# Kernel tuning notes

Measured on AMD Instinct MI355X. Metric: run time of the kernel, lower is better.

The kernel has to match this reference:

```python
import jax, jax.numpy as jnp
import numpy as np


def maxpool2x2(x):
    # NCHW 2x2 max pool, stride 2
    return jax.lax.reduce_window(x, -jnp.inf, jax.lax.max, (1, 1, 2, 2), (1, 1, 2, 2), 'VALID')


def _xavier_uniform(k, shape):
    fan_out, fan_in = shape
    lim = np.sqrt(6.0 / (fan_in + fan_out))
    return jax.random.uniform(k, shape, jnp.float32, -lim, lim)


def setup_inputs() -> dict:
    key = jax.random.key(0)
    ks = jax.random.split(key, 5)
    C = 64
    x = jax.random.normal(ks[0], (4, C, 128, 128), jnp.float32)
    Wq = _xavier_uniform(ks[1], (C // 8, C))  # 1x1 conv == channel matmul
    Wk = _xavier_uniform(ks[2], (C // 8, C))
    Wv = _xavier_uniform(ks[3], (C // 2, C))
    Wo = _xavier_uniform(ks[4], (C, C // 2))
    gamma = jnp.full((1,), 0.1, jnp.float32)  # nonzero so attention branch contributes
    return {"x": x, "Wq": Wq, "Wk": Wk, "Wv": Wv, "Wo": Wo, "gamma": gamma}


def reference(x, Wq, Wk, Wv, Wo, gamma):
    b, c, w, h = x.shape
    # 1x1 convs as channel contractions
    q = jnp.einsum('oc,bchw->bohw', Wq, x).reshape(b, c // 8, w * h)          # [b, c/8, k]
    k_ = maxpool2x2(jnp.einsum('oc,bchw->bohw', Wk, x)).reshape(b, c // 8, -1)  # [b, c/8, f]
    v = maxpool2x2(jnp.einsum('oc,bchw->bohw', Wv, x)).reshape(b, c // 2, -1)   # [b, c/2, f]
    # softmax over full-resolution query positions k (last axis), per pooled position f
    weights = jax.nn.softmax(jnp.einsum('bcf,bck->bfk', k_, q), axis=-1)        # [b, f, k]
    out = jnp.einsum('bcf,bfk->bck', v, weights).reshape(b, c // 2, w, h)       # [b, c/2, w, h]
    out = jnp.einsum('oc,bchw->bohw', Wo, out)                                   # [b, c, w, h]
    return gamma * out + x
```

## Files before the change

### kernel.cpp

```cpp
#include <hip/hip_runtime.h>
#include <cstdint>
#include <cstddef>


#define LOG2E 1.44269504088896340736f

typedef __attribute__((ext_vector_type(8)))  __bf16 bf8_t;
typedef __attribute__((ext_vector_type(16))) float  fx16;

__device__ __forceinline__ unsigned short f2bf(float f) {
  unsigned int u = __builtin_bit_cast(unsigned int, f);
  u += 0x7FFFu + ((u >> 16) & 1u);
  return (unsigned short)(u >> 16);
}
__device__ __forceinline__ unsigned int pk2(unsigned short lo, unsigned short hi) {
  return (unsigned int)lo | ((unsigned int)hi << 16);
}
__device__ __forceinline__ int pi16(int s) {
  int m = (s >> 2) & 3;
  return (m == 1 || m == 2) ? (s ^ 12) : s;
}

#if __has_builtin(__builtin_amdgcn_exp2f)
#define EXP2F __builtin_amdgcn_exp2f
#else
#define EXP2F exp2f
#endif

__global__ void __launch_bounds__(256) k_qkv(const float* __restrict__ x,
                                             const float* __restrict__ Wq,
                                             const float* __restrict__ Wk,
                                             const float* __restrict__ Wv,
                                             unsigned short* __restrict__ Qp,
                                             unsigned short* __restrict__ KpB,
                                             float* __restrict__ Vp) {
  __shared__ float wq[64][8], wk[64][8], wv[64][32];
  int t = threadIdx.x;
  for (int i = t; i < 512; i += 256) {
    wq[i & 63][i >> 6] = Wq[i];
    wk[i & 63][i >> 6] = Wk[i];
  }
  for (int i = t; i < 2048; i += 256) wv[i & 63][i >> 6] = Wv[i];
  __syncthreads();
  int gid = blockIdx.x * 256 + t;
  int b = gid >> 14, r = gid & 16383, f = r >> 2, pos = r & 3;
  int p0 = ((f >> 6) << 1) | (pos >> 1);
  int p1 = ((f & 63) << 1) | (pos & 1);
  int k = p0 * 128 + p1;
  const float* xp = x + (size_t)b * (64 * 16384) + k;
  float q[8], kc[8], vc[32];
#pragma unroll
  for (int o = 0; o < 8; ++o) { q[o] = 0.f; kc[o] = 0.f; }
#pragma unroll
  for (int o = 0; o < 32; ++o) vc[o] = 0.f;
  for (int c = 0; c < 64; ++c) {
    float xv = xp[(size_t)c * 16384];
    const float4* q4 = reinterpret_cast<const float4*>(&wq[c][0]);
    const float4* k4 = reinterpret_cast<const float4*>(&wk[c][0]);
    const float4* v4 = reinterpret_cast<const float4*>(&wv[c][0]);
#pragma unroll
    for (int j = 0; j < 2; ++j) {
      float4 a = q4[j], bq = k4[j];
      q[4 * j]      += a.x * xv; q[4 * j + 1]  += a.y * xv;
      q[4 * j + 2]  += a.z * xv; q[4 * j + 3]  += a.w * xv;
      kc[4 * j]     += bq.x * xv; kc[4 * j + 1] += bq.y * xv;
      kc[4 * j + 2] += bq.z * xv; kc[4 * j + 3] += bq.w * xv;
    }
#pragma unroll
    for (int j = 0; j < 8; ++j) {
      float4 a = v4[j];
      vc[4 * j]     += a.x * xv; vc[4 * j + 1] += a.y * xv;
      vc[4 * j + 2] += a.z * xv; vc[4 * j + 3] += a.w * xv;
    }
  }
  unsigned short q16[8];
#pragma unroll
  for (int o = 0; o < 8; ++o) q16[o] = f2bf(q[o]);
  uint4 qa, z4;
  qa.x = pk2(q16[0], q16[1]); qa.y = pk2(q16[2], q16[3]);
  qa.z = pk2(q16[4], q16[5]); qa.w = pk2(q16[6], q16[7]);
  z4.x = z4.y = z4.z = z4.w = 0u;
  uint4* qdst = reinterpret_cast<uint4*>(Qp + ((size_t)b * 16384 + k) * 16);
  qdst[0] = qa; qdst[1] = z4;
#pragma unroll
  for (int o = 0; o < 8; ++o) {
    kc[o] = fmaxf(kc[o], __shfl_xor(kc[o], 1));
    kc[o] = fmaxf(kc[o], __shfl_xor(kc[o], 2));
  }
#pragma unroll
  for (int o = 0; o < 32; ++o) {
    vc[o] = fmaxf(vc[o], __shfl_xor(vc[o], 1));
    vc[o] = fmaxf(vc[o], __shfl_xor(vc[o], 2));
  }
  if (pos == 0) {
    size_t idx = (size_t)b * 4096 + f;
    unsigned short k16[8];
#pragma unroll
    for (int o = 0; o < 8; ++o) k16[o] = f2bf(kc[o] * LOG2E);
    uint4 ka;
    ka.x = pk2(k16[0], k16[1]); ka.y = pk2(k16[2], k16[3]);
    ka.z = pk2(k16[4], k16[5]); ka.w = pk2(k16[6], k16[7]);
    uint4* kdst = reinterpret_cast<uint4*>(KpB + idx * 16);
    kdst[0] = ka; kdst[1] = z4;
    float4* vdst = reinterpret_cast<float4*>(Vp + idx * 32);
#pragma unroll
    for (int j = 0; j < 8; ++j)
      vdst[j] = make_float4(vc[4 * j], vc[4 * j + 1], vc[4 * j + 2], vc[4 * j + 3]);
  }
}

__global__ void __launch_bounds__(1024) k_lsum(const unsigned short* __restrict__ Qp,
                                               const unsigned short* __restrict__ KpB,
                                               float* __restrict__ Ls) {
  int b = blockIdx.x >> 6, g = blockIdx.x & 63;
  int wv = threadIdx.x >> 6, lane = threadIdx.x & 63;
  int half = lane >> 5, l31 = lane & 31;
  const unsigned short* kb =
      KpB + ((size_t)(b * 4096 + g * 64 + l31)) * 16 + half * 8;
  bf8_t A0 = *reinterpret_cast<const bf8_t*>(kb);
  bf8_t A1 = *reinterpret_cast<const bf8_t*>(kb + 32 * 16);
  const unsigned short* qbase = Qp + ((size_t)b * 16384) * 16 + half * 8;
  fx16 z;
#pragma unroll
  for (int i = 0; i < 16; ++i) z[i] = 0.f;
  float l[32];
#pragma unroll
  for (int i = 0; i < 32; ++i) l[i] = 0.f;
  int t0 = wv * 32;
  bf8_t B = *reinterpret_cast<const bf8_t*>(qbase + (size_t)(t0 * 32 + l31) * 16);
  for (int i = 0; i < 32; ++i) {
    int tn = t0 + ((i + 1) & 31);
    bf8_t nB = *reinterpret_cast<const bf8_t*>(qbase + (size_t)(tn * 32 + l31) * 16);
    fx16 s0 = __builtin_amdgcn_mfma_f32_32x32x16_bf16(A0, B, z, 0, 0, 0);
    fx16 s1 = __builtin_amdgcn_mfma_f32_32x32x16_bf16(A1, B, z, 0, 0, 0);
#pragma unroll
    for (int r0 = 0; r0 < 16; ++r0) l[r0] += EXP2F(s0[r0]);
#pragma unroll
    for (int r0 = 0; r0 < 16; ++r0) l[16 + r0] += EXP2F(s1[r0]);
    B = nB;
  }
#pragma unroll
  for (int r0 = 0; r0 < 32; ++r0)
    for (int d = 1; d < 32; d <<= 1) l[r0] += __shfl_xor(l[r0], d);
  __shared__ float sl[16][2][32];
  if (l31 == 0) {
#pragma unroll
    for (int r0 = 0; r0 < 16; ++r0) {
      int row = (r0 & 3) + 8 * (r0 >> 2) + 4 * half;
      sl[wv][0][row] = l[r0];
      sl[wv][1][row] = l[16 + r0];
    }
  }
  __syncthreads();
  if (threadIdx.x < 64) {
    int fgi = threadIdx.x >> 5, row = threadIdx.x & 31;
    float L = 0.f;
#pragma unroll
    for (int w2 = 0; w2 < 16; ++w2) L += sl[w2][fgi][row];
    Ls[(size_t)b * 4096 + g * 64 + fgi * 32 + row] = L;
  }
}

__global__ void __launch_bounds__(256) k_pack(const float* __restrict__ Vp,
                                              const float* __restrict__ Ls,
                                              const float* __restrict__ Wo,
                                              unsigned short* __restrict__ Vpp,
                                              unsigned short* __restrict__ Wop) {
  if (blockIdx.x == 64) {
    for (int i = threadIdx.x; i < 2048; i += 256) {
      int c = i & 31;
      Wop[i] = f2bf(Wo[(i & ~31) | (c & 16) | pi16(c & 15)]);
    }
    return;
  }
  int b = blockIdx.x >> 4, f0 = (blockIdx.x & 15) * 256;
  __shared__ unsigned short T[32][264];
  int t = threadIdx.x;
  float rl = 1.0f / Ls[(size_t)b * 4096 + f0 + t];
  const float* vp = Vp + ((size_t)b * 4096 + f0 + t) * 32;
  int fl = (t & ~15) | pi16(t & 15);
  for (int c = 0; c < 32; ++c) T[c][fl] = f2bf(vp[c] * rl);
  __syncthreads();
  for (int u = t; u < 1024; u += 256) {
    int row = u >> 5, e0 = (u & 31) * 8;
    uint4 val = *reinterpret_cast<const uint4*>(&T[row][e0]);
    *reinterpret_cast<uint4*>(Vpp + ((size_t)b * 32 + row) * 4096 + f0 + e0) = val;
  }
}

__global__ void __launch_bounds__(256) k_attn(const unsigned short* __restrict__ Qp,
                                              const unsigned short* __restrict__ KpB,
                                              const unsigned short* __restrict__ Vpp,
                                              const unsigned short* __restrict__ Wop,
                                              const float* __restrict__ x,
                                              const float* __restrict__ gamma,
                                              float* __restrict__ out) {
  int b = blockIdx.x >> 8, kp = blockIdx.x & 255;
  int wv = threadIdx.x >> 6, lane = threadIdx.x & 63;
  int half = lane >> 5, l31 = lane & 31;
  int kbase = kp * 64;
  const unsigned short* qb = Qp + ((size_t)b * 16384 + kbase + l31) * 16 + half * 8;
  bf8_t Bq0 = *reinterpret_cast<const bf8_t*>(qb);
  bf8_t Bq1 = *reinterpret_cast<const bf8_t*>(qb + 32 * 16);
  fx16 z;
#pragma unroll
  for (int i = 0; i < 16; ++i) z[i] = 0.f;
  fx16 acc0 = z, acc1 = z;
  const unsigned short* kpB = KpB + ((size_t)b * 4096 + l31) * 16 + half * 8;
  const unsigned short* vpB = Vpp + ((size_t)(b * 32 + l31)) * 4096 + half * 8;
  int c0 = wv * 32;
  int f0 = c0 * 32;
  bf8_t Ak  = *reinterpret_cast<const bf8_t*>(kpB + (size_t)f0 * 16);
  bf8_t Av0 = *reinterpret_cast<const bf8_t*>(vpB + f0);
  bf8_t Av1 = *reinterpret_cast<const bf8_t*>(vpB + f0 + 16);
  for (int fc = 0; fc < 32; ++fc) {
    int f1 = (c0 + ((fc + 1) & 31)) * 32;
    bf8_t nAk  = *reinterpret_cast<const bf8_t*>(kpB + (size_t)f1 * 16);
    bf8_t nAv0 = *reinterpret_cast<const bf8_t*>(vpB + f1);
    bf8_t nAv1 = *reinterpret_cast<const bf8_t*>(vpB + f1 + 16);
    fx16 s0 = __builtin_amdgcn_mfma_f32_32x32x16_bf16(Ak, Bq0, z, 0, 0, 0);
    fx16 s1 = __builtin_amdgcn_mfma_f32_32x32x16_bf16(Ak, Bq1, z, 0, 0, 0);
    bf8_t P00, P01, P10, P11;
#pragma unroll
    for (int j = 0; j < 8; ++j) {
      P00[j] = (__bf16)EXP2F(s0[j]);
      P01[j] = (__bf16)EXP2F(s0[8 + j]);
    }
#pragma unroll
    for (int j = 0; j < 8; ++j) {
      P10[j] = (__bf16)EXP2F(s1[j]);
      P11[j] = (__bf16)EXP2F(s1[8 + j]);
    }
    acc0 = __builtin_amdgcn_mfma_f32_32x32x16_bf16(Av0, P00, acc0, 0, 0, 0);
    acc1 = __builtin_amdgcn_mfma_f32_32x32x16_bf16(Av0, P10, acc1, 0, 0, 0);
    acc0 = __builtin_amdgcn_mfma_f32_32x32x16_bf16(Av1, P01, acc0, 0, 0, 0);
    acc1 = __builtin_amdgcn_mfma_f32_32x32x16_bf16(Av1, P11, acc1, 0, 0, 0);
    Ak = nAk; Av0 = nAv0; Av1 = nAv1;
  }
  __shared__ float sacc[4][2][4][64][4];
#pragma unroll
  for (int j4 = 0; j4 < 4; ++j4) {
    *reinterpret_cast<float4*>(&sacc[wv][0][j4][lane][0]) =
        make_float4(acc0[4 * j4], acc0[4 * j4 + 1], acc0[4 * j4 + 2], acc0[4 * j4 + 3]);
    *reinterpret_cast<float4*>(&sacc[wv][1][j4][lane][0]) =
        make_float4(acc1[4 * j4], acc1[4 * j4 + 1], acc1[4 * j4 + 2], acc1[4 * j4 + 3]);
  }
  __syncthreads();
  int kt = wv & 1, ot = wv >> 1;
  fx16 tot;
#pragma unroll
  for (int j4 = 0; j4 < 4; ++j4) {
    float4 a0 = *reinterpret_cast<const float4*>(&sacc[0][kt][j4][lane][0]);
    float4 a1 = *reinterpret_cast<const float4*>(&sacc[1][kt][j4][lane][0]);
    float4 a2 = *reinterpret_cast<const float4*>(&sacc[2][kt][j4][lane][0]);
    float4 a3 = *reinterpret_cast<const float4*>(&sacc[3][kt][j4][lane][0]);
    tot[4 * j4]     = (a0.x + a1.x) + (a2.x + a3.x);
    tot[4 * j4 + 1] = (a0.y + a1.y) + (a2.y + a3.y);
    tot[4 * j4 + 2] = (a0.z + a1.z) + (a2.z + a3.z);
    tot[4 * j4 + 3] = (a0.w + a1.w) + (a2.w + a3.w);
  }
  bf8_t Ob0, Ob1;
#pragma unroll
  for (int j = 0; j < 8; ++j) { Ob0[j] = (__bf16)tot[j]; Ob1[j] = (__bf16)tot[8 + j]; }
  const unsigned short* wb = Wop + (ot * 32 + l31) * 32 + half * 8;
  bf8_t Aw0 = *reinterpret_cast<const bf8_t*>(wb);
  bf8_t Aw1 = *reinterpret_cast<const bf8_t*>(wb + 16);
  fx16 y = __builtin_amdgcn_mfma_f32_32x32x16_bf16(Aw0, Ob0, z, 0, 0, 0);
  y = __builtin_amdgcn_mfma_f32_32x32x16_bf16(Aw1, Ob1, y, 0, 0, 0);
  float g = gamma[0];
  int k = kbase + kt * 32 + l31;
  const float* xp = x + (size_t)b * 64 * 16384 + k;
  float* op = out + (size_t)b * 64 * 16384 + k;
#pragma unroll
  for (int r0 = 0; r0 < 16; ++r0) {
    int row = (r0 & 3) + 8 * (r0 >> 2) + 4 * half + ot * 32;
    op[(size_t)row * 16384] = fmaf(g, y[r0], xp[(size_t)row * 16384]);
  }
}

extern "C" void kernel_launch(void* const* d_in, const int* in_sizes, int n_in,
                              void* d_out, int out_size, void* d_ws, size_t ws_size,
                              hipStream_t stream) {
  const float* x     = (const float*)d_in[0];
  const float* Wq    = (const float*)d_in[1];
  const float* Wk    = (const float*)d_in[2];
  const float* Wv    = (const float*)d_in[3];
  const float* Wo    = (const float*)d_in[4];
  const float* gamma = (const float*)d_in[5];
  float* out = (float*)d_out;
  char* ws = (char*)d_ws;
  unsigned short* Qp  = (unsigned short*)(ws + 0);
  unsigned short* KpB = (unsigned short*)(ws + 2097152);
  float*          Vp  = (float*)(ws + 2621440);
  unsigned short* Vpp = (unsigned short*)(ws + 4718592);
  float*          Ls  = (float*)(ws + 5767168);
  unsigned short* Wop = (unsigned short*)(ws + 5832704);

  k_qkv <<<dim3(256),  dim3(256),  0, stream>>>(x, Wq, Wk, Wv, Qp, KpB, Vp);
  k_lsum<<<dim3(256),  dim3(1024), 0, stream>>>(Qp, KpB, Ls);
  k_pack<<<dim3(65),   dim3(256),  0, stream>>>(Vp, Ls, Wo, Vpp, Wop);
  k_attn<<<dim3(1024), dim3(256),  0, stream>>>(Qp, KpB, Vpp, Wop, x, gamma, out);
}
```

Before: 168.0 us.

## Retile QKV projection, fold V packing into lsum, double attn waves

The QKV projection kernel is rewritten to stage x tiles in shared memory, with each thread computing 12 output channels for a 2x2 pooling window so the max-pool is done in registers instead of with shuffles. The Wo packing moves into an extra block of that kernel. V normalization and transposition are fused into the lsum kernel, which removes the separate pack kernel and the Ls buffer. The attention kernel now runs 8 waves per block, each covering half the f-chunks, and reduces the partial sums through shared memory. This cuts launches and global round trips and adds parallelism per block, at the cost of an extra LDS reduction step and higher register pressure in the projection kernel.

```diff
diff --git a/kernel.cpp b/kernel.cpp
--- a/kernel.cpp
+++ b/kernel.cpp
@@ -19,6 +19,9 @@
 __device__ __forceinline__ int pi16(int s) {
   int m = (s >> 2) & 3;
   return (m == 1 || m == 2) ? (s ^ 12) : s;
+}
+__device__ __forceinline__ float max4(const float* a) {
+  return fmaxf(fmaxf(a[0], a[1]), fmaxf(a[2], a[3]));
 }
 
 #if __has_builtin(__builtin_amdgcn_exp2f)
@@ -31,87 +34,101 @@
                                              const float* __restrict__ Wq,
                                              const float* __restrict__ Wk,
                                              const float* __restrict__ Wv,
+                                             const float* __restrict__ Wo,
                                              unsigned short* __restrict__ Qp,
                                              unsigned short* __restrict__ KpB,
-                                             float* __restrict__ Vp) {
-  __shared__ float wq[64][8], wk[64][8], wv[64][32];
+                                             float* __restrict__ Vp,
+                                             unsigned short* __restrict__ Wop) {
+  if (blockIdx.x == 256) {
+    for (int i = threadIdx.x; i < 2048; i += 256) {
+      int c = i & 31;
+      Wop[i] = f2bf(Wo[(i & ~31) | (c & 16) | pi16(c & 15)]);
+    }
+    return;
+  }
+  __shared__ float ws[48][64];
+  __shared__ float xs[16][256];
   int t = threadIdx.x;
   for (int i = t; i < 512; i += 256) {
-    wq[i & 63][i >> 6] = Wq[i];
-    wk[i & 63][i >> 6] = Wk[i];
-  }
-  for (int i = t; i < 2048; i += 256) wv[i & 63][i >> 6] = Wv[i];
-  __syncthreads();
-  int gid = blockIdx.x * 256 + t;
-  int b = gid >> 14, r = gid & 16383, f = r >> 2, pos = r & 3;
-  int p0 = ((f >> 6) << 1) | (pos >> 1);
-  int p1 = ((f & 63) << 1) | (pos & 1);
-  int k = p0 * 128 + p1;
-  const float* xp = x + (size_t)b * (64 * 16384) + k;
-  float q[8], kc[8], vc[32];
-#pragma unroll
-  for (int o = 0; o < 8; ++o) { q[o] = 0.f; kc[o] = 0.f; }
-#pragma unroll
-  for (int o = 0; o < 32; ++o) vc[o] = 0.f;
-  for (int c = 0; c < 64; ++c) {
-    float xv = xp[(size_t)c * 16384];
-    const float4* q4 = reinterpret_cast<const float4*>(&wq[c][0]);
-    const float4* k4 = reinterpret_cast<const float4*>(&wk[c][0]);
-    const float4* v4 = reinterpret_cast<const float4*>(&wv[c][0]);
-#pragma unroll
-    for (int j = 0; j < 2; ++j) {
-      float4 a = q4[j], bq = k4[j];
-      q[4 * j]      += a.x * xv; q[4 * j + 1]  += a.y * xv;
-      q[4 * j + 2]  += a.z * xv; q[4 * j + 3]  += a.w * xv;
-      kc[4 * j]     += bq.x * xv; kc[4 * j + 1] += bq.y * xv;
-      kc[4 * j + 2] += bq.z * xv; kc[4 * j + 3] += bq.w * xv;
-    }
-#pragma unroll
-    for (int j = 0; j < 8; ++j) {
-      float4 a = v4[j];
-      vc[4 * j]     += a.x * xv; vc[4 * j + 1] += a.y * xv;
-      vc[4 * j + 2] += a.z * xv; vc[4 * j + 3] += a.w * xv;
-    }
-  }
-  unsigned short q16[8];
-#pragma unroll
-  for (int o = 0; o < 8; ++o) q16[o] = f2bf(q[o]);
-  uint4 qa, z4;
-  qa.x = pk2(q16[0], q16[1]); qa.y = pk2(q16[2], q16[3]);
-  qa.z = pk2(q16[4], q16[5]); qa.w = pk2(q16[6], q16[7]);
-  z4.x = z4.y = z4.z = z4.w = 0u;
-  uint4* qdst = reinterpret_cast<uint4*>(Qp + ((size_t)b * 16384 + k) * 16);
-  qdst[0] = qa; qdst[1] = z4;
-#pragma unroll
-  for (int o = 0; o < 8; ++o) {
-    kc[o] = fmaxf(kc[o], __shfl_xor(kc[o], 1));
-    kc[o] = fmaxf(kc[o], __shfl_xor(kc[o], 2));
-  }
-#pragma unroll
-  for (int o = 0; o < 32; ++o) {
-    vc[o] = fmaxf(vc[o], __shfl_xor(vc[o], 1));
-    vc[o] = fmaxf(vc[o], __shfl_xor(vc[o], 2));
-  }
-  if (pos == 0) {
-    size_t idx = (size_t)b * 4096 + f;
-    unsigned short k16[8];
-#pragma unroll
-    for (int o = 0; o < 8; ++o) k16[o] = f2bf(kc[o] * LOG2E);
-    uint4 ka;
-    ka.x = pk2(k16[0], k16[1]); ka.y = pk2(k16[2], k16[3]);
-    ka.z = pk2(k16[4], k16[5]); ka.w = pk2(k16[6], k16[7]);
-    uint4* kdst = reinterpret_cast<uint4*>(KpB + idx * 16);
-    kdst[0] = ka; kdst[1] = z4;
-    float4* vdst = reinterpret_cast<float4*>(Vp + idx * 32);
-#pragma unroll
-    for (int j = 0; j < 8; ++j)
-      vdst[j] = make_float4(vc[4 * j], vc[4 * j + 1], vc[4 * j + 2], vc[4 * j + 3]);
+    ws[i >> 6][i & 63] = Wq[i];
+    ws[8 + (i >> 6)][i & 63] = Wk[i];
+  }
+  for (int i = t; i < 2048; i += 256) ws[16 + (i >> 6)][i & 63] = Wv[i];
+  int b = blockIdx.x >> 6, frow = blockIdx.x & 63;
+  int rg = t >> 6, fc = t & 63;
+  const float* xb = x + (size_t)b * (64 * 16384) + frow * 256;
+  float acc[12][4];
+#pragma unroll
+  for (int j = 0; j < 12; ++j)
+#pragma unroll
+    for (int p = 0; p < 4; ++p) acc[j][p] = 0.f;
+  int cl = t >> 4, seg = t & 15;
+  for (int cc = 0; cc < 4; ++cc) {
+    __syncthreads();
+    const float4* src =
+        reinterpret_cast<const float4*>(xb + (size_t)(cc * 16 + cl) * 16384 + seg * 16);
+    float4* dst = reinterpret_cast<float4*>(&xs[cl][seg * 16]);
+#pragma unroll
+    for (int j = 0; j < 4; ++j) dst[j] = src[j];
+    __syncthreads();
+#pragma unroll
+    for (int c16 = 0; c16 < 16; ++c16) {
+      int c = cc * 16 + c16;
+      float2 xa = *reinterpret_cast<const float2*>(&xs[c16][2 * fc]);
+      float2 xbv = *reinterpret_cast<const float2*>(&xs[c16][128 + 2 * fc]);
+#pragma unroll
+      for (int j = 0; j < 12; ++j) {
+        float w = ws[12 * rg + j][c];
+        acc[j][0] = fmaf(w, xa.x, acc[j][0]);
+        acc[j][1] = fmaf(w, xa.y, acc[j][1]);
+        acc[j][2] = fmaf(w, xbv.x, acc[j][2]);
+        acc[j][3] = fmaf(w, xbv.y, acc[j][3]);
+      }
+    }
+  }
+  size_t idx = (size_t)b * 4096 + frow * 64 + fc;
+  uint4 z4; z4.x = z4.y = z4.z = z4.w = 0u;
+  if (rg == 0) {
+#pragma unroll
+    for (int p = 0; p < 4; ++p) {
+      int kpos = frow * 256 + (p >> 1) * 128 + 2 * fc + (p & 1);
+      uint4 qa;
+      qa.x = pk2(f2bf(acc[0][p]), f2bf(acc[1][p]));
+      qa.y = pk2(f2bf(acc[2][p]), f2bf(acc[3][p]));
+      qa.z = pk2(f2bf(acc[4][p]), f2bf(acc[5][p]));
+      qa.w = pk2(f2bf(acc[6][p]), f2bf(acc[7][p]));
+      uint4* qdst = reinterpret_cast<uint4*>(Qp + ((size_t)b * 16384 + kpos) * 16);
+      qdst[0] = qa; qdst[1] = z4;
+    }
+    uint2 kw;
+    kw.x = pk2(f2bf(max4(acc[8]) * LOG2E), f2bf(max4(acc[9]) * LOG2E));
+    kw.y = pk2(f2bf(max4(acc[10]) * LOG2E), f2bf(max4(acc[11]) * LOG2E));
+    *reinterpret_cast<uint2*>(KpB + idx * 16) = kw;
+  } else if (rg == 1) {
+    uint2 kw;
+    kw.x = pk2(f2bf(max4(acc[0]) * LOG2E), f2bf(max4(acc[1]) * LOG2E));
+    kw.y = pk2(f2bf(max4(acc[2]) * LOG2E), f2bf(max4(acc[3]) * LOG2E));
+    *reinterpret_cast<uint2*>(KpB + idx * 16 + 4) = kw;
+    *reinterpret_cast<uint4*>(KpB + idx * 16 + 8) = z4;
+    float* vd = Vp + idx * 32;
+    *reinterpret_cast<float4*>(vd) =
+        make_float4(max4(acc[4]), max4(acc[5]), max4(acc[6]), max4(acc[7]));
+    *reinterpret_cast<float4*>(vd + 4) =
+        make_float4(max4(acc[8]), max4(acc[9]), max4(acc[10]), max4(acc[11]));
+  } else {
+    float* vd = Vp + idx * 32 + (rg == 2 ? 8 : 20);
+#pragma unroll
+    for (int j4 = 0; j4 < 3; ++j4)
+      *reinterpret_cast<float4*>(vd + 4 * j4) =
+          make_float4(max4(acc[4 * j4]), max4(acc[4 * j4 + 1]),
+                      max4(acc[4 * j4 + 2]), max4(acc[4 * j4 + 3]));
   }
 }
 
 __global__ void __launch_bounds__(1024) k_lsum(const unsigned short* __restrict__ Qp,
                                                const unsigned short* __restrict__ KpB,
-                                               float* __restrict__ Ls) {
+                                               const float* __restrict__ Vp,
+                                               unsigned short* __restrict__ Vpp) {
   int b = blockIdx.x >> 6, g = blockIdx.x & 63;
   int wv = threadIdx.x >> 6, lane = threadIdx.x & 63;
   int half = lane >> 5, l31 = lane & 31;
@@ -143,6 +160,8 @@
   for (int r0 = 0; r0 < 32; ++r0)
     for (int d = 1; d < 32; d <<= 1) l[r0] += __shfl_xor(l[r0], d);
   __shared__ float sl[16][2][32];
+  __shared__ float Linv[64];
+  __shared__ unsigned short Tv[32][72];
   if (l31 == 0) {
 #pragma unroll
     for (int r0 = 0; r0 < 16; ++r0) {
@@ -157,38 +176,29 @@
     float L = 0.f;
 #pragma unroll
     for (int w2 = 0; w2 < 16; ++w2) L += sl[w2][fgi][row];
-    Ls[(size_t)b * 4096 + g * 64 + fgi * 32 + row] = L;
-  }
-}
-
-__global__ void __launch_bounds__(256) k_pack(const float* __restrict__ Vp,
-                                              const float* __restrict__ Ls,
-                                              const float* __restrict__ Wo,
-                                              unsigned short* __restrict__ Vpp,
-                                              unsigned short* __restrict__ Wop) {
-  if (blockIdx.x == 64) {
-    for (int i = threadIdx.x; i < 2048; i += 256) {
-      int c = i & 31;
-      Wop[i] = f2bf(Wo[(i & ~31) | (c & 16) | pi16(c & 15)]);
-    }
-    return;
-  }
-  int b = blockIdx.x >> 4, f0 = (blockIdx.x & 15) * 256;
-  __shared__ unsigned short T[32][264];
-  int t = threadIdx.x;
-  float rl = 1.0f / Ls[(size_t)b * 4096 + f0 + t];
-  const float* vp = Vp + ((size_t)b * 4096 + f0 + t) * 32;
-  int fl = (t & ~15) | pi16(t & 15);
-  for (int c = 0; c < 32; ++c) T[c][fl] = f2bf(vp[c] * rl);
-  __syncthreads();
-  for (int u = t; u < 1024; u += 256) {
-    int row = u >> 5, e0 = (u & 31) * 8;
-    uint4 val = *reinterpret_cast<const uint4*>(&T[row][e0]);
-    *reinterpret_cast<uint4*>(Vpp + ((size_t)b * 32 + row) * 4096 + f0 + e0) = val;
-  }
-}
-
-__global__ void __launch_bounds__(256) k_attn(const unsigned short* __restrict__ Qp,
+    Linv[threadIdx.x] = 1.0f / L;
+  }
+  __syncthreads();
+  if (threadIdx.x < 512) {
+    int floc = threadIdx.x >> 3, c4 = (threadIdx.x & 7) * 4;
+    float4 v = *reinterpret_cast<const float4*>(
+        Vp + ((size_t)(b * 4096 + g * 64 + floc)) * 32 + c4);
+    float s = Linv[floc];
+    int dst = (floc & ~15) | pi16(floc & 15);
+    Tv[c4][dst]     = f2bf(v.x * s);
+    Tv[c4 + 1][dst] = f2bf(v.y * s);
+    Tv[c4 + 2][dst] = f2bf(v.z * s);
+    Tv[c4 + 3][dst] = f2bf(v.w * s);
+  }
+  __syncthreads();
+  if (threadIdx.x < 256) {
+    int c = threadIdx.x >> 3, u = threadIdx.x & 7;
+    uint4 val = *reinterpret_cast<const uint4*>(&Tv[c][u * 8]);
+    *reinterpret_cast<uint4*>(Vpp + ((size_t)(b * 32 + c)) * 4096 + g * 64 + u * 8) = val;
+  }
+}
+
+__global__ void __launch_bounds__(512) k_attn(const unsigned short* __restrict__ Qp,
                                               const unsigned short* __restrict__ KpB,
                                               const unsigned short* __restrict__ Vpp,
                                               const unsigned short* __restrict__ Wop,
@@ -208,13 +218,13 @@
   fx16 acc0 = z, acc1 = z;
   const unsigned short* kpB = KpB + ((size_t)b * 4096 + l31) * 16 + half * 8;
   const unsigned short* vpB = Vpp + ((size_t)(b * 32 + l31)) * 4096 + half * 8;
-  int c0 = wv * 32;
+  int c0 = wv * 16;
   int f0 = c0 * 32;
   bf8_t Ak  = *reinterpret_cast<const bf8_t*>(kpB + (size_t)f0 * 16);
   bf8_t Av0 = *reinterpret_cast<const bf8_t*>(vpB + f0);
   bf8_t Av1 = *reinterpret_cast<const bf8_t*>(vpB + f0 + 16);
-  for (int fc = 0; fc < 32; ++fc) {
-    int f1 = (c0 + ((fc + 1) & 31)) * 32;
+  for (int fc = 0; fc < 16; ++fc) {
+    int f1 = (c0 + ((fc + 1) & 15)) * 32;
     bf8_t nAk  = *reinterpret_cast<const bf8_t*>(kpB + (size_t)f1 * 16);
     bf8_t nAv0 = *reinterpret_cast<const bf8_t*>(vpB + f1);
     bf8_t nAv1 = *reinterpret_cast<const bf8_t*>(vpB + f1 + 16);
@@ -238,14 +248,32 @@
     Ak = nAk; Av0 = nAv0; Av1 = nAv1;
   }
   __shared__ float sacc[4][2][4][64][4];
-#pragma unroll
-  for (int j4 = 0; j4 < 4; ++j4) {
-    *reinterpret_cast<float4*>(&sacc[wv][0][j4][lane][0]) =
-        make_float4(acc0[4 * j4], acc0[4 * j4 + 1], acc0[4 * j4 + 2], acc0[4 * j4 + 3]);
-    *reinterpret_cast<float4*>(&sacc[wv][1][j4][lane][0]) =
-        make_float4(acc1[4 * j4], acc1[4 * j4 + 1], acc1[4 * j4 + 2], acc1[4 * j4 + 3]);
-  }
-  __syncthreads();
+  if (wv >= 4) {
+    int s = wv - 4;
+#pragma unroll
+    for (int j4 = 0; j4 < 4; ++j4) {
+      *reinterpret_cast<float4*>(&sacc[s][0][j4][lane][0]) =
+          make_float4(acc0[4 * j4], acc0[4 * j4 + 1], acc0[4 * j4 + 2], acc0[4 * j4 + 3]);
+      *reinterpret_cast<float4*>(&sacc[s][1][j4][lane][0]) =
+          make_float4(acc1[4 * j4], acc1[4 * j4 + 1], acc1[4 * j4 + 2], acc1[4 * j4 + 3]);
+    }
+  }
+  __syncthreads();
+  if (wv < 4) {
+#pragma unroll
+    for (int j4 = 0; j4 < 4; ++j4) {
+      float4 p0 = *reinterpret_cast<const float4*>(&sacc[wv][0][j4][lane][0]);
+      float4 p1 = *reinterpret_cast<const float4*>(&sacc[wv][1][j4][lane][0]);
+      p0.x += acc0[4 * j4]; p0.y += acc0[4 * j4 + 1];
+      p0.z += acc0[4 * j4 + 2]; p0.w += acc0[4 * j4 + 3];
+      p1.x += acc1[4 * j4]; p1.y += acc1[4 * j4 + 1];
+      p1.z += acc1[4 * j4 + 2]; p1.w += acc1[4 * j4 + 3];
+      *reinterpret_cast<float4*>(&sacc[wv][0][j4][lane][0]) = p0;
+      *reinterpret_cast<float4*>(&sacc[wv][1][j4][lane][0]) = p1;
+    }
+  }
+  __syncthreads();
+  if (wv >= 4) return;
   int kt = wv & 1, ot = wv >> 1;
   fx16 tot;
 #pragma unroll
@@ -293,11 +321,9 @@
   unsigned short* KpB = (unsigned short*)(ws + 2097152);
   float*          Vp  = (float*)(ws + 2621440);
   unsigned short* Vpp = (unsigned short*)(ws + 4718592);
-  float*          Ls  = (float*)(ws + 5767168);
-  unsigned short* Wop = (unsigned short*)(ws + 5832704);
-
-  k_qkv <<<dim3(256),  dim3(256),  0, stream>>>(x, Wq, Wk, Wv, Qp, KpB, Vp);
-  k_lsum<<<dim3(256),  dim3(1024), 0, stream>>>(Qp, KpB, Ls);
-  k_pack<<<dim3(65),   dim3(256),  0, stream>>>(Vp, Ls, Wo, Vpp, Wop);
-  k_attn<<<dim3(1024), dim3(256),  0, stream>>>(Qp, KpB, Vpp, Wop, x, gamma, out);
-}
+  unsigned short* Wop = (unsigned short*)(ws + 5767168);
+
+  k_qkv <<<dim3(257),  dim3(256),  0, stream>>>(x, Wq, Wk, Wv, Wo, Qp, KpB, Vp, Wop);
+  k_lsum<<<dim3(256),  dim3(1024), 0, stream>>>(Qp, KpB, Vp, Vpp);
+  k_attn<<<dim3(1024), dim3(512),  0, stream>>>(Qp, KpB, Vpp, Wop, x, gamma, out);
+}
```

Measured after the change: 149.8 us. 1.12x faster.
